# Performance work log

Measured on AMD Instinct MI355X. Metric: run time of the kernel, lower is better.

## Reference

```python
import jax, jax.numpy as jnp
import numpy as np

H = 64  # hidden_size
IN = 6  # input_size


def _uniform(key, shape, bound):
    return jax.random.uniform(key, shape, jnp.float32, -bound, bound)


def setup_inputs() -> dict:
    key = jax.random.key(0)
    ks = jax.random.split(key, 20)
    B, T = 1024, 512
    bnd = 1.0 / np.sqrt(H)  # PyTorch LSTM/Linear default init scale
    inp = {"x": jax.random.normal(ks[0], (B, T, IN), jnp.float32)}
    # LSTM params, PyTorch layout: w_ih [4H, in], w_hh [4H, H], gate order i,f,g,o
    in_sizes = [IN, H, H]
    for l in range(3):
        inp[f"w_ih{l}"] = _uniform(ks[1 + 4 * l], (4 * H, in_sizes[l]), bnd)
        inp[f"w_hh{l}"] = _uniform(ks[2 + 4 * l], (4 * H, H), bnd)
        inp[f"b_ih{l}"] = _uniform(ks[3 + 4 * l], (4 * H,), bnd)
        inp[f"b_hh{l}"] = _uniform(ks[4 + 4 * l], (4 * H,), bnd)
    # MLP head: fc1 (64->128), fc3 (128->64), fc2 (64->2)
    inp["fc1_w"] = _uniform(ks[13], (128, H), 1.0 / np.sqrt(H))
    inp["fc1_b"] = _uniform(ks[14], (128,), 1.0 / np.sqrt(H))
    inp["fc3_w"] = _uniform(ks[15], (64, 128), 1.0 / np.sqrt(128))
    inp["fc3_b"] = _uniform(ks[16], (64,), 1.0 / np.sqrt(128))
    inp["fc2_w"] = _uniform(ks[17], (2, 64), 1.0 / np.sqrt(64))
    inp["fc2_b"] = _uniform(ks[18], (2,), 1.0 / np.sqrt(64))
    return inp


def _lstm_layer(x, w_ih, w_hh, b_ih, b_hh):
    # x: [B, T, F] -> [B, T, H]; zero initial state, PyTorch gate order i,f,g,o
    B = x.shape[0]
    # Precompute input projections for all timesteps (one big GEMM)
    xg = jnp.einsum('btf,gf->btg', x, w_ih) + b_ih + b_hh  # [B, T, 4H]

    def step(carry, xt):
        h, c = carry
        gates = xt + h @ w_hh.T
        i, f, g, o = jnp.split(gates, 4, axis=-1)
        c = jax.nn.sigmoid(f) * c + jax.nn.sigmoid(i) * jnp.tanh(g)
        h = jax.nn.sigmoid(o) * jnp.tanh(c)
        return (h, c), h

    h0 = jnp.zeros((B, H), x.dtype)
    (_, _), ys = jax.lax.scan(step, (h0, h0), jnp.swapaxes(xg, 0, 1))
    return jnp.swapaxes(ys, 0, 1)


def reference(x, w_ih0, w_hh0, b_ih0, b_hh0, w_ih1, w_hh1, b_ih1, b_hh1,
              w_ih2, w_hh2, b_ih2, b_hh2, fc1_w, fc1_b, fc3_w, fc3_b, fc2_w, fc2_b):
    h = _lstm_layer(x, w_ih0, w_hh0, b_ih0, b_hh0)
    h = _lstm_layer(h, w_ih1, w_hh1, b_ih1, b_hh1)
    h = _lstm_layer(h, w_ih2, w_hh2, b_ih2, b_hh2)
    z = h[:, -1, :]  # last timestep: [B, H]
    z = jax.nn.relu(z @ fc1_w.T + fc1_b)
    z = jax.nn.relu(z @ fc3_w.T + fc3_b)
    return z @ fc2_w.T + fc2_b  # [B, 2]
```

## Files before the change

kernel.cpp:

```cpp
#include <hip/hip_runtime.h>
#include <cstdint>
#include <cstddef>

namespace {

constexpr int B_ = 1024;
constexpr int T_ = 512;
constexpr int H_ = 64;
constexpr int NG = 64;
constexpr int D_RING = 64;
constexpr int CP = 16;
constexpr int SLOT_BYTES = 16 * 64 * 2;

constexpr float L2E  = 1.4426950408889634f;

typedef short bf16x8 __attribute__((ext_vector_type(8)));
typedef float f32x4  __attribute__((ext_vector_type(4)));

__device__ __forceinline__ float exp2_hw(float x) {
    float r; asm("v_exp_f32 %0, %1" : "=v"(r) : "v"(x)); return r;
}
__device__ __forceinline__ float rcp_hw(float x) {
    float r; asm("v_rcp_f32 %0, %1" : "=v"(r) : "v"(x)); return r;
}

__device__ __forceinline__ unsigned short f2bf(float f) {
    unsigned u = __float_as_uint(f);
    u += 0x7FFF + ((u >> 16) & 1);
    return (unsigned short)(u >> 16);
}

__device__ __forceinline__ unsigned cvtpk_bf16(float a, float b) {
    unsigned r;
    asm("v_cvt_pk_bf16_f32 %0, %1, %2" : "=v"(r) : "v"(a), "v"(b));
    return r;
}

__device__ __forceinline__ void lds_barrier() {
    asm volatile("s_waitcnt lgkmcnt(0)\n\ts_barrier" ::: "memory");
}

__device__ __forceinline__ void ring_store16(void* dst, bf16x8 v) {
    asm volatile("global_store_dwordx4 %0, %1, off sc0 sc1"
                 :: "v"(dst), "v"(v) : "memory");
}
__device__ __forceinline__ int flag_load(const int* p) {
    int v;
    asm volatile("global_load_dword %0, %1, off sc0 sc1\n\t"
                 "s_waitcnt vmcnt(0)" : "=v"(v) : "v"(p) : "memory");
    return v;
}
__device__ __forceinline__ void flag_store_drain(int* p, int v) {
    asm volatile("s_waitcnt vmcnt(0)\n\t"
                 "global_store_dword %0, %1, off sc0 sc1"
                 :: "v"(p), "v"(v) : "memory");
}
__device__ __forceinline__ void flag_store(int* p, int v) {
    asm volatile("global_store_dword %0, %1, off sc0 sc1"
                 :: "v"(p), "v"(v) : "memory");
}
__device__ __forceinline__ void spin_ge(const int* p, int tgt) {
    while (flag_load(p) < tgt) __builtin_amdgcn_s_sleep(1);
}

__global__ void init_flags(int* p, int n) {
    int i = blockIdx.x * 256 + threadIdx.x;
    if (i < n) p[i] = -1;
}

__global__ void cvt_bf16_kernel(const float* __restrict__ src,
                                unsigned short* __restrict__ dst, int n) {
    int i = blockIdx.x * 256 + threadIdx.x;
    if (i < n) {
        int row = i >> 6;
        float sc = ((row >> 6) == 2) ? 2.0f * L2E : L2E;
        dst[i] = f2bf(src[i] * sc);
    }
}

__global__ void cvt_wih0_kernel(const float* __restrict__ src,
                                unsigned short* __restrict__ dst) {
    int i = blockIdx.x * 256 + threadIdx.x;
    int g = i >> 3, k = i & 7;
    float sc = ((g >> 6) == 2) ? 2.0f * L2E : L2E;
    dst[i] = (k < 6) ? f2bf(src[g * 6 + k] * sc) : (unsigned short)0;
}

__global__ void build_xpk(const float* __restrict__ x,
                          unsigned short* __restrict__ xPk) {
    int idx = blockIdx.x * 256 + threadIdx.x;
    int k = idx & 7, r = (idx >> 3) & 15, g = (idx >> 7) & 63, t = idx >> 13;
    float v = (k < 6) ? x[((size_t)(g * 16 + r) * T_ + t) * 6 + k] : 0.f;
    xPk[idx] = f2bf(v);
}

template<int LAY>
__device__ __forceinline__ void pipe_body(
    int g,
    const unsigned short* __restrict__ xPk,
    const unsigned short* __restrict__ wih,
    const unsigned short* __restrict__ whh,
    const float* __restrict__ bih, const float* __restrict__ bhh,
    const unsigned short* __restrict__ ringIn, unsigned short* __restrict__ ringOut,
    const int* progIn, int* progOut, int* consInP, const int* consOutP,
    float* __restrict__ hlast, unsigned short* lds)
{
    const int tid = threadIdx.x;
    const int l   = tid & 63;
    const int w   = tid >> 6;
    const int r16 = l & 15;
    const int kq  = l >> 4;
    const int hdim = w * 16 + r16;

    bf16x8 whh_f[4][2], wih_f[4][2];
    f32x4  bias_acc[4];
    #pragma unroll
    for (int d = 0; d < 4; ++d) {
        const int gg = d * 64 + hdim;
        const float sc = (d == 2) ? 2.0f * L2E : L2E;
        const float b = (bih[gg] + bhh[gg]) * sc;
        bias_acc[d] = f32x4{b, b, b, b};
        whh_f[d][0] = *(const bf16x8*)(whh + gg * 64 + kq * 8);
        whh_f[d][1] = *(const bf16x8*)(whh + gg * 64 + 32 + kq * 8);
        if constexpr (LAY == 0) {
            bf16x8 z = {};
            wih_f[d][0] = (kq == 0) ? *(const bf16x8*)(wih + gg * 8) : z;
            wih_f[d][1] = z;
        } else {
            wih_f[d][0] = *(const bf16x8*)(wih + gg * 64 + kq * 8);
            wih_f[d][1] = *(const bf16x8*)(wih + gg * 64 + 32 + kq * 8);
        }
    }

    char* ldsb = (char*)lds;
    const int rdA0 = r16 * 128 + (((0 + kq) ^ (r16 & 7)) << 4);
    const int rdA1 = r16 * 128 + (((4 + kq) ^ (r16 & 7)) << 4);
    int wrA[4];
    #pragma unroll
    for (int r = 0; r < 4; ++r) {
        const int row = 4 * kq + r;
        wrA[r] = row * 128 + (((hdim >> 3) ^ (row & 7)) << 4) + (hdim & 7) * 2;
    }
    const int rOffA = r16 * 128 + kq * 16;
    const int rOffB = r16 * 128 + 64 + kq * 16;

    auto xrow = [&](int t) -> const char* {
        return (const char*)xPk + (((size_t)t * NG + g) * 16 + r16) * 16;
    };

    ((uint4*)ldsb)[tid] = make_uint4(0, 0, 0, 0);
    float c[4] = {0.f, 0.f, 0.f, 0.f};
    lds_barrier();

    bf16x8 cur0 = {}, cur1 = {};
    f32x4 accA[4], accB[4];
    {
        bf16x8 x0a = {}, x0b = {};
        if constexpr (LAY > 0) {
            spin_ge(progIn, (CP - 1 < T_ - 1) ? CP - 1 : T_ - 1);
            const char* s0 = (const char*)ringIn;
            const char* s1 = (const char*)ringIn + SLOT_BYTES;
            asm volatile(
                "global_load_dwordx4 %0, %4, off sc0 sc1\n\t"
                "global_load_dwordx4 %1, %5, off sc0 sc1\n\t"
                "global_load_dwordx4 %2, %6, off sc0 sc1\n\t"
                "global_load_dwordx4 %3, %7, off sc0 sc1\n\t"
                "s_waitcnt vmcnt(0)"
                : "=v"(x0a), "=v"(x0b), "=v"(cur0), "=v"(cur1)
                : "v"(s0 + rOffA), "v"(s0 + rOffB), "v"(s1 + rOffA), "v"(s1 + rOffB)
                : "memory");
            __builtin_amdgcn_sched_barrier(0);
        } else {
            asm volatile(
                "global_load_dwordx4 %0, %2, off\n\t"
                "global_load_dwordx4 %1, %3, off\n\t"
                "s_waitcnt vmcnt(0)"
                : "=v"(x0a), "=v"(cur0)
                : "v"(xrow(0)), "v"(xrow(1))
                : "memory");
            __builtin_amdgcn_sched_barrier(0);
        }
        #pragma unroll
        for (int d = 0; d < 4; ++d) {
            accA[d] = __builtin_amdgcn_mfma_f32_16x16x32_bf16(x0a, wih_f[d][0], bias_acc[d], 0, 0, 0);
            if constexpr (LAY != 0)
                accA[d] = __builtin_amdgcn_mfma_f32_16x16x32_bf16(x0b, wih_f[d][1], accA[d], 0, 0, 0);
        }
    }

    auto step = [&](int t, int par, f32x4* accC, f32x4* accN) {
        if constexpr (LAY < 2) {
            if ((t & (CP - 1)) == 0) spin_ge(consOutP, t + CP - D_RING);
        }
        if constexpr (LAY < 2) {
            if ((t & (CP - 1)) == 1 && t > 1) {
                if (tid == 0) flag_store_drain(progOut, t - 2);
            }
        }

        const bf16x8 ha = *(const bf16x8*)(ldsb + ((par ^ 1) << 11) + rdA0);
        const bf16x8 hb = *(const bf16x8*)(ldsb + ((par ^ 1) << 11) + rdA1);

        #pragma unroll
        for (int d = 0; d < 4; ++d) {
            accC[d] = __builtin_amdgcn_mfma_f32_16x16x32_bf16(ha, whh_f[d][0], accC[d], 0, 0, 0);
            accC[d] = __builtin_amdgcn_mfma_f32_16x16x32_bf16(hb, whh_f[d][1], accC[d], 0, 0, 0);
        }

        if constexpr (LAY < 2) {
            if (w == 0) asm volatile("s_waitcnt vmcnt(2)" ::: "memory");
            else        asm volatile("s_waitcnt vmcnt(0)" ::: "memory");
        } else {
            asm volatile("s_waitcnt vmcnt(0)" ::: "memory");
        }
        __builtin_amdgcn_sched_barrier(0);

        if (t + 1 < T_) {
            #pragma unroll
            for (int d = 0; d < 4; ++d) {
                accN[d] = __builtin_amdgcn_mfma_f32_16x16x32_bf16(cur0, wih_f[d][0], bias_acc[d], 0, 0, 0);
                if constexpr (LAY != 0)
                    accN[d] = __builtin_amdgcn_mfma_f32_16x16x32_bf16(cur1, wih_f[d][1], accN[d], 0, 0, 0);
            }
        }

        {
            const int s = t + 2;
            if (s < T_) {
                if constexpr (LAY > 0) {
                    if ((s & (CP - 1)) == 0) {
                        int tgt = s + CP - 1; if (tgt > T_ - 1) tgt = T_ - 1;
                        spin_ge(progIn, tgt);
                    }
                    const char* src = (const char*)ringIn + (s & (D_RING - 1)) * SLOT_BYTES;
                    asm volatile(
                        "global_load_dwordx4 %0, %2, off sc0 sc1\n\t"
                        "global_load_dwordx4 %1, %3, off sc0 sc1"
                        : "=v"(cur0), "=v"(cur1)
                        : "v"(src + rOffA), "v"(src + rOffB)
                        : "memory");
                } else {
                    asm volatile("global_load_dwordx4 %0, %1, off"
                                 : "=v"(cur0) : "v"(xrow(s)) : "memory");
                }
            }
        }

        if constexpr (LAY < 2) {
            if (w == 0) {
                char* dst = (char*)ringOut + ((t - 1) & (D_RING - 1)) * SLOT_BYTES;
                ring_store16(dst + rOffA, ha);
                ring_store16(dst + rOffB, hb);
            }
        }

        float h[4];
        #pragma unroll
        for (int r = 0; r < 4; ++r) {
            const float gi = accC[0][r], gf = accC[1][r], gg = accC[2][r], go = accC[3][r];
            const float si = rcp_hw(1.0f + exp2_hw(-gi));
            const float sf = rcp_hw(1.0f + exp2_hw(-gf));
            const float so = rcp_hw(1.0f + exp2_hw(-go));
            const float tg = __builtin_fmaf(2.0f, rcp_hw(1.0f + exp2_hw(-gg)), -1.0f);
            c[r] = sf * c[r] + si * tg;
            const float tc = __builtin_fmaf(2.0f, rcp_hw(1.0f + exp2_hw(c[r] * (-2.0f * L2E))), -1.0f);
            h[r] = so * tc;
        }
        const unsigned p01 = cvtpk_bf16(h[0], h[1]);
        const unsigned p23 = cvtpk_bf16(h[2], h[3]);
        char* wbase = ldsb + (par << 11);
        *(unsigned short*)(wbase + wrA[0]) = (unsigned short)(p01 & 0xffff);
        *(unsigned short*)(wbase + wrA[1]) = (unsigned short)(p01 >> 16);
        *(unsigned short*)(wbase + wrA[2]) = (unsigned short)(p23 & 0xffff);
        *(unsigned short*)(wbase + wrA[3]) = (unsigned short)(p23 >> 16);
        if constexpr (LAY == 2) {
            if (t == T_ - 1) {
                #pragma unroll
                for (int r = 0; r < 4; ++r)
                    hlast[(g * 16 + kq * 4 + r) * 64 + hdim] = h[r];
            }
        }

        lds_barrier();

        if constexpr (LAY > 0) {
            if (tid == 0 && (t & (CP - 1)) == CP - 1) flag_store(consInP, t);
        }
    };

    #pragma unroll 1
    for (int t = 0; t < T_; t += 2) {
        step(t,     0, accA, accB);
        step(t + 1, 1, accB, accA);
    }

    if constexpr (LAY < 2) {
        if (w == 0) {
            const int par = (T_ - 1) & 1;
            const bf16x8 ha = *(const bf16x8*)(ldsb + (par << 11) + rdA0);
            const bf16x8 hb = *(const bf16x8*)(ldsb + (par << 11) + rdA1);
            char* dst = (char*)ringOut + ((T_ - 1) & (D_RING - 1)) * SLOT_BYTES;
            ring_store16(dst + rOffA, ha);
            ring_store16(dst + rOffB, hb);
        }
        lds_barrier();
        if (tid == 0) flag_store_drain(progOut, T_ - 1);
    }
}

__global__ __launch_bounds__(256, 1)
void lstm_pipe(const unsigned short* __restrict__ xPk,
               const unsigned short* __restrict__ wih0p,
               const unsigned short* __restrict__ wih1,
               const unsigned short* __restrict__ wih2,
               const unsigned short* __restrict__ whh0,
               const unsigned short* __restrict__ whh1,
               const unsigned short* __restrict__ whh2,
               const float* __restrict__ bih0, const float* __restrict__ bhh0,
               const float* __restrict__ bih1, const float* __restrict__ bhh1,
               const float* __restrict__ bih2, const float* __restrict__ bhh2,
               unsigned short* __restrict__ ring, int* __restrict__ flags,
               float* __restrict__ hlast)
{
    __shared__ unsigned short lds[2][1024];

    const int g   = blockIdx.x & 63;
    const int lay = blockIdx.x >> 6;

    const size_t GSHORTS = (size_t)D_RING * SLOT_BYTES / 2;
    unsigned short* r0 = ring + ((size_t)0 * NG + g) * GSHORTS;
    unsigned short* r1 = ring + ((size_t)1 * NG + g) * GSHORTS;
    int* prog0 = flags + (0 * 64 + g) * 16;
    int* prog1 = flags + (1 * 64 + g) * 16;
    int* cons0 = flags + (128 + 0 * 64 + g) * 16;
    int* cons1 = flags + (128 + 1 * 64 + g) * 16;

    if (lay == 0) {
        pipe_body<0>(g, xPk, wih0p, whh0, bih0, bhh0,
                     nullptr, r0, nullptr, prog0, nullptr, cons0,
                     hlast, &lds[0][0]);
    } else if (lay == 1) {
        pipe_body<1>(g, xPk, wih1, whh1, bih1, bhh1,
                     r0, r1, prog0, prog1, cons0, cons1,
                     hlast, &lds[0][0]);
    } else {
        pipe_body<2>(g, xPk, wih2, whh2, bih2, bhh2,
                     r1, nullptr, prog1, nullptr, cons1, nullptr,
                     hlast, &lds[0][0]);
    }
}

__global__ __launch_bounds__(128)
void mlp_head_kernel(const float* __restrict__ hlast,
                     const float* __restrict__ fc1_w, const float* __restrict__ fc1_b,
                     const float* __restrict__ fc3_w, const float* __restrict__ fc3_b,
                     const float* __restrict__ fc2_w, const float* __restrict__ fc2_b,
                     float* __restrict__ outp)
{
    __shared__ float s_h[H_];
    __shared__ float s_z1[128];
    __shared__ float s_z3[64];
    const int b = blockIdx.x, tid = threadIdx.x;

    if (tid < H_) s_h[tid] = hlast[b * H_ + tid];
    __syncthreads();

    {
        float acc = fc1_b[tid];
        #pragma unroll
        for (int k = 0; k < H_; ++k) acc += fc1_w[tid * H_ + k] * s_h[k];
        s_z1[tid] = fmaxf(acc, 0.0f);
    }
    __syncthreads();

    if (tid < 64) {
        float acc = fc3_b[tid];
        #pragma unroll
        for (int k = 0; k < 128; ++k) acc += fc3_w[tid * 128 + k] * s_z1[k];
        s_z3[tid] = fmaxf(acc, 0.0f);
    }
    __syncthreads();

    if (tid < 2) {
        float acc = fc2_b[tid];
        #pragma unroll
        for (int k = 0; k < 64; ++k) acc += fc2_w[tid * 64 + k] * s_z3[k];
        outp[b * 2 + tid] = acc;
    }
}

}

extern "C" void kernel_launch(void* const* d_in, const int* in_sizes, int n_in,
                              void* d_out, int out_size, void* d_ws, size_t ws_size,
                              hipStream_t stream) {
    (void)in_sizes; (void)n_in; (void)out_size; (void)ws_size;

    const float* x     = (const float*)d_in[0];
    const float* wih0  = (const float*)d_in[1];
    const float* whh0  = (const float*)d_in[2];
    const float* bih0  = (const float*)d_in[3];
    const float* bhh0  = (const float*)d_in[4];
    const float* wih1  = (const float*)d_in[5];
    const float* whh1  = (const float*)d_in[6];
    const float* bih1  = (const float*)d_in[7];
    const float* bhh1  = (const float*)d_in[8];
    const float* wih2  = (const float*)d_in[9];
    const float* whh2  = (const float*)d_in[10];
    const float* bih2  = (const float*)d_in[11];
    const float* bhh2  = (const float*)d_in[12];
    const float* fc1_w = (const float*)d_in[13];
    const float* fc1_b = (const float*)d_in[14];
    const float* fc3_w = (const float*)d_in[15];
    const float* fc3_b = (const float*)d_in[16];
    const float* fc2_w = (const float*)d_in[17];
    const float* fc2_b = (const float*)d_in[18];
    float* out = (float*)d_out;

    char* base = (char*)d_ws;
    const size_t RING_B = (size_t)2 * NG * D_RING * SLOT_BYTES;
    const size_t XPK_B  = (size_t)T_ * NG * 16 * 8 * 2;
    const size_t FLAG_B = 4096 * sizeof(int);
    unsigned short* ring  = (unsigned short*)(base);
    unsigned short* xPk   = (unsigned short*)(base + RING_B);
    int*            flags = (int*)(base + RING_B + XPK_B);
    float*          hlast = (float*)(base + RING_B + XPK_B + FLAG_B);
    char* wp = base + RING_B + XPK_B + FLAG_B + (size_t)B_ * H_ * 4;
    unsigned short* whh_b[3];
    for (int i = 0; i < 3; ++i) { whh_b[i] = (unsigned short*)wp; wp += 256 * 64 * 2; }
    unsigned short* wih_b1 = (unsigned short*)wp; wp += 256 * 64 * 2;
    unsigned short* wih_b2 = (unsigned short*)wp; wp += 256 * 64 * 2;
    unsigned short* wih0p  = (unsigned short*)wp; wp += 256 * 8 * 2;

    init_flags<<<16, 256, 0, stream>>>(flags, 4096);
    const int NW = 256 * 64;
    cvt_bf16_kernel<<<NW / 256, 256, 0, stream>>>(whh0, whh_b[0], NW);
    cvt_bf16_kernel<<<NW / 256, 256, 0, stream>>>(whh1, whh_b[1], NW);
    cvt_bf16_kernel<<<NW / 256, 256, 0, stream>>>(whh2, whh_b[2], NW);
    cvt_bf16_kernel<<<NW / 256, 256, 0, stream>>>(wih1, wih_b1, NW);
    cvt_bf16_kernel<<<NW / 256, 256, 0, stream>>>(wih2, wih_b2, NW);
    cvt_wih0_kernel<<<8, 256, 0, stream>>>(wih0, wih0p);
    build_xpk<<<(T_ * NG * 16 * 8) / 256, 256, 0, stream>>>(x, xPk);

    lstm_pipe<<<192, 256, 0, stream>>>(xPk, wih0p, wih_b1, wih_b2,
                                       whh_b[0], whh_b[1], whh_b[2],
                                       bih0, bhh0, bih1, bhh1, bih2, bhh2,
                                       ring, flags, hlast);

    mlp_head_kernel<<<B_, 128, 0, stream>>>(hlast, fc1_w, fc1_b, fc3_w, fc3_b,
                                            fc2_w, fc2_b, out);
}
```

Before: 393.1 us.

## Fuse three LSTM layers into one wavefront-pipelined block per batch group

Replaces the 192-block cross-block pipeline, in which each layer ran on its own block and passed hidden states through a global-memory ring guarded by spin flags, with 64 blocks that each run all three layers. The layers are skewed by one timestep and hand off hidden states through LDS tiles. This removes global ring traffic, flag polling and the flag-init kernel. In exchange each block does three layers' worth of MFMA and activation work serially per step, which lengthens the per-step critical path, and only 64 CUs are used. Register pressure also rises because all three layers' weights are held in registers.

New measurement: 793.5 us. +101.8%, slower.

```diff
diff --git a/kernel.cpp b/kernel.cpp
--- a/kernel.cpp
+++ b/kernel.cpp
@@ -8,9 +8,6 @@
 constexpr int T_ = 512;
 constexpr int H_ = 64;
 constexpr int NG = 64;
-constexpr int D_RING = 64;
-constexpr int CP = 16;
-constexpr int SLOT_BYTES = 16 * 64 * 2;
 
 constexpr float L2E  = 1.4426950408889634f;
 
@@ -40,33 +37,6 @@
     asm volatile("s_waitcnt lgkmcnt(0)\n\ts_barrier" ::: "memory");
 }
 
-__device__ __forceinline__ void ring_store16(void* dst, bf16x8 v) {
-    asm volatile("global_store_dwordx4 %0, %1, off sc0 sc1"
-                 :: "v"(dst), "v"(v) : "memory");
-}
-__device__ __forceinline__ int flag_load(const int* p) {
-    int v;
-    asm volatile("global_load_dword %0, %1, off sc0 sc1\n\t"
-                 "s_waitcnt vmcnt(0)" : "=v"(v) : "v"(p) : "memory");
-    return v;
-}
-__device__ __forceinline__ void flag_store_drain(int* p, int v) {
-    asm volatile("s_waitcnt vmcnt(0)\n\t"
-                 "global_store_dword %0, %1, off sc0 sc1"
-                 :: "v"(p), "v"(v) : "memory");
-}
-__device__ __forceinline__ void flag_store(int* p, int v) {
-    asm volatile("global_store_dword %0, %1, off sc0 sc1"
-                 :: "v"(p), "v"(v) : "memory");
-}
-__device__ __forceinline__ void spin_ge(const int* p, int tgt) {
-    while (flag_load(p) < tgt) __builtin_amdgcn_s_sleep(1);
-}
-
-__global__ void init_flags(int* p, int n) {
-    int i = blockIdx.x * 256 + threadIdx.x;
-    if (i < n) p[i] = -1;
-}
 
 __global__ void cvt_bf16_kernel(const float* __restrict__ src,
                                 unsigned short* __restrict__ dst, int n) {
@@ -94,17 +64,22 @@
     xPk[idx] = f2bf(v);
 }
 
-template<int LAY>
-__device__ __forceinline__ void pipe_body(
-    int g,
-    const unsigned short* __restrict__ xPk,
-    const unsigned short* __restrict__ wih,
-    const unsigned short* __restrict__ whh,
-    const float* __restrict__ bih, const float* __restrict__ bhh,
-    const unsigned short* __restrict__ ringIn, unsigned short* __restrict__ ringOut,
-    const int* progIn, int* progOut, int* consInP, const int* consOutP,
-    float* __restrict__ hlast, unsigned short* lds)
+__global__ __launch_bounds__(256, 1)
+void lstm_fused(const unsigned short* __restrict__ xPk,
+                const unsigned short* __restrict__ wih0p,
+                const unsigned short* __restrict__ wih1,
+                const unsigned short* __restrict__ wih2,
+                const unsigned short* __restrict__ whh0,
+                const unsigned short* __restrict__ whh1,
+                const unsigned short* __restrict__ whh2,
+                const float* __restrict__ bih0, const float* __restrict__ bhh0,
+                const float* __restrict__ bih1, const float* __restrict__ bhh1,
+                const float* __restrict__ bih2, const float* __restrict__ bhh2,
+                float* __restrict__ hlast)
 {
+    __shared__ unsigned short lds[6][1024];
+
+    const int g   = blockIdx.x;
     const int tid = threadIdx.x;
     const int l   = tid & 63;
     const int w   = tid >> 6;
@@ -112,24 +87,34 @@
     const int kq  = l >> 4;
     const int hdim = w * 16 + r16;
 
-    bf16x8 whh_f[4][2], wih_f[4][2];
-    f32x4  bias_acc[4];
+    bf16x8 w0h[4][2], w0x[4];
+    bf16x8 w1h[4][2], w1x[4][2];
+    bf16x8 w2h[4][2], w2x[4][2];
+    f32x4  b0[4], b1[4], b2[4];
     #pragma unroll
     for (int d = 0; d < 4; ++d) {
         const int gg = d * 64 + hdim;
         const float sc = (d == 2) ? 2.0f * L2E : L2E;
-        const float b = (bih[gg] + bhh[gg]) * sc;
-        bias_acc[d] = f32x4{b, b, b, b};
-        whh_f[d][0] = *(const bf16x8*)(whh + gg * 64 + kq * 8);
-        whh_f[d][1] = *(const bf16x8*)(whh + gg * 64 + 32 + kq * 8);
-        if constexpr (LAY == 0) {
+        const float v0 = (bih0[gg] + bhh0[gg]) * sc;
+        const float v1 = (bih1[gg] + bhh1[gg]) * sc;
+        const float v2 = (bih2[gg] + bhh2[gg]) * sc;
+        b0[d] = f32x4{v0, v0, v0, v0};
+        b1[d] = f32x4{v1, v1, v1, v1};
+        b2[d] = f32x4{v2, v2, v2, v2};
+        w0h[d][0] = *(const bf16x8*)(whh0 + gg * 64 + kq * 8);
+        w0h[d][1] = *(const bf16x8*)(whh0 + gg * 64 + 32 + kq * 8);
+        w1h[d][0] = *(const bf16x8*)(whh1 + gg * 64 + kq * 8);
+        w1h[d][1] = *(const bf16x8*)(whh1 + gg * 64 + 32 + kq * 8);
+        w2h[d][0] = *(const bf16x8*)(whh2 + gg * 64 + kq * 8);
+        w2h[d][1] = *(const bf16x8*)(whh2 + gg * 64 + 32 + kq * 8);
+        {
             bf16x8 z = {};
-            wih_f[d][0] = (kq == 0) ? *(const bf16x8*)(wih + gg * 8) : z;
-            wih_f[d][1] = z;
-        } else {
-            wih_f[d][0] = *(const bf16x8*)(wih + gg * 64 + kq * 8);
-            wih_f[d][1] = *(const bf16x8*)(wih + gg * 64 + 32 + kq * 8);
-        }
+            w0x[d] = (kq == 0) ? *(const bf16x8*)(wih0p + gg * 8) : z;
+        }
+        w1x[d][0] = *(const bf16x8*)(wih1 + gg * 64 + kq * 8);
+        w1x[d][1] = *(const bf16x8*)(wih1 + gg * 64 + 32 + kq * 8);
+        w2x[d][0] = *(const bf16x8*)(wih2 + gg * 64 + kq * 8);
+        w2x[d][1] = *(const bf16x8*)(wih2 + gg * 64 + 32 + kq * 8);
     }
 
     char* ldsb = (char*)lds;
@@ -141,123 +126,32 @@
         const int row = 4 * kq + r;
         wrA[r] = row * 128 + (((hdim >> 3) ^ (row & 7)) << 4) + (hdim & 7) * 2;
     }
-    const int rOffA = r16 * 128 + kq * 16;
-    const int rOffB = r16 * 128 + 64 + kq * 16;
-
-    auto xrow = [&](int t) -> const char* {
-        return (const char*)xPk + (((size_t)t * NG + g) * 16 + r16) * 16;
-    };
-
-    ((uint4*)ldsb)[tid] = make_uint4(0, 0, 0, 0);
-    float c[4] = {0.f, 0.f, 0.f, 0.f};
+    auto tile = [&](int layer, int p) -> char* {
+        return ldsb + (size_t)(layer * 2 + p) * 2048;
+    };
+
+    {
+        uint4* z = (uint4*)ldsb;
+        z[tid] = make_uint4(0, 0, 0, 0);
+        z[tid + 256] = make_uint4(0, 0, 0, 0);
+        z[tid + 512] = make_uint4(0, 0, 0, 0);
+    }
+    float c0[4] = {0.f, 0.f, 0.f, 0.f};
+    float c1[4] = {0.f, 0.f, 0.f, 0.f};
+    float c2[4] = {0.f, 0.f, 0.f, 0.f};
     lds_barrier();
 
-    bf16x8 cur0 = {}, cur1 = {};
-    f32x4 accA[4], accB[4];
-    {
-        bf16x8 x0a = {}, x0b = {};
-        if constexpr (LAY > 0) {
-            spin_ge(progIn, (CP - 1 < T_ - 1) ? CP - 1 : T_ - 1);
-            const char* s0 = (const char*)ringIn;
-            const char* s1 = (const char*)ringIn + SLOT_BYTES;
-            asm volatile(
-                "global_load_dwordx4 %0, %4, off sc0 sc1\n\t"
-                "global_load_dwordx4 %1, %5, off sc0 sc1\n\t"
-                "global_load_dwordx4 %2, %6, off sc0 sc1\n\t"
-                "global_load_dwordx4 %3, %7, off sc0 sc1\n\t"
-                "s_waitcnt vmcnt(0)"
-                : "=v"(x0a), "=v"(x0b), "=v"(cur0), "=v"(cur1)
-                : "v"(s0 + rOffA), "v"(s0 + rOffB), "v"(s1 + rOffA), "v"(s1 + rOffB)
-                : "memory");
-            __builtin_amdgcn_sched_barrier(0);
-        } else {
-            asm volatile(
-                "global_load_dwordx4 %0, %2, off\n\t"
-                "global_load_dwordx4 %1, %3, off\n\t"
-                "s_waitcnt vmcnt(0)"
-                : "=v"(x0a), "=v"(cur0)
-                : "v"(xrow(0)), "v"(xrow(1))
-                : "memory");
-            __builtin_amdgcn_sched_barrier(0);
-        }
-        #pragma unroll
-        for (int d = 0; d < 4; ++d) {
-            accA[d] = __builtin_amdgcn_mfma_f32_16x16x32_bf16(x0a, wih_f[d][0], bias_acc[d], 0, 0, 0);
-            if constexpr (LAY != 0)
-                accA[d] = __builtin_amdgcn_mfma_f32_16x16x32_bf16(x0b, wih_f[d][1], accA[d], 0, 0, 0);
-        }
-    }
-
-    auto step = [&](int t, int par, f32x4* accC, f32x4* accN) {
-        if constexpr (LAY < 2) {
-            if ((t & (CP - 1)) == 0) spin_ge(consOutP, t + CP - D_RING);
-        }
-        if constexpr (LAY < 2) {
-            if ((t & (CP - 1)) == 1 && t > 1) {
-                if (tid == 0) flag_store_drain(progOut, t - 2);
-            }
-        }
-
-        const bf16x8 ha = *(const bf16x8*)(ldsb + ((par ^ 1) << 11) + rdA0);
-        const bf16x8 hb = *(const bf16x8*)(ldsb + ((par ^ 1) << 11) + rdA1);
-
-        #pragma unroll
-        for (int d = 0; d < 4; ++d) {
-            accC[d] = __builtin_amdgcn_mfma_f32_16x16x32_bf16(ha, whh_f[d][0], accC[d], 0, 0, 0);
-            accC[d] = __builtin_amdgcn_mfma_f32_16x16x32_bf16(hb, whh_f[d][1], accC[d], 0, 0, 0);
-        }
-
-        if constexpr (LAY < 2) {
-            if (w == 0) asm volatile("s_waitcnt vmcnt(2)" ::: "memory");
-            else        asm volatile("s_waitcnt vmcnt(0)" ::: "memory");
-        } else {
-            asm volatile("s_waitcnt vmcnt(0)" ::: "memory");
-        }
-        __builtin_amdgcn_sched_barrier(0);
-
-        if (t + 1 < T_) {
-            #pragma unroll
-            for (int d = 0; d < 4; ++d) {
-                accN[d] = __builtin_amdgcn_mfma_f32_16x16x32_bf16(cur0, wih_f[d][0], bias_acc[d], 0, 0, 0);
-                if constexpr (LAY != 0)
-                    accN[d] = __builtin_amdgcn_mfma_f32_16x16x32_bf16(cur1, wih_f[d][1], accN[d], 0, 0, 0);
-            }
-        }
-
-        {
-            const int s = t + 2;
-            if (s < T_) {
-                if constexpr (LAY > 0) {
-                    if ((s & (CP - 1)) == 0) {
-                        int tgt = s + CP - 1; if (tgt > T_ - 1) tgt = T_ - 1;
-                        spin_ge(progIn, tgt);
-                    }
-                    const char* src = (const char*)ringIn + (s & (D_RING - 1)) * SLOT_BYTES;
-                    asm volatile(
-                        "global_load_dwordx4 %0, %2, off sc0 sc1\n\t"
-                        "global_load_dwordx4 %1, %3, off sc0 sc1"
-                        : "=v"(cur0), "=v"(cur1)
-                        : "v"(src + rOffA), "v"(src + rOffB)
-                        : "memory");
-                } else {
-                    asm volatile("global_load_dwordx4 %0, %1, off"
-                                 : "=v"(cur0) : "v"(xrow(s)) : "memory");
-                }
-            }
-        }
-
-        if constexpr (LAY < 2) {
-            if (w == 0) {
-                char* dst = (char*)ringOut + ((t - 1) & (D_RING - 1)) * SLOT_BYTES;
-                ring_store16(dst + rOffA, ha);
-                ring_store16(dst + rOffB, hb);
-            }
-        }
-
-        float h[4];
+    constexpr size_t XSTEP = (size_t)NG * 16 * 16;
+    const char* xp0 = (const char*)xPk + ((size_t)g * 16 + r16) * 16;
+    const char* xpA = xp0;
+    const char* xpB = xp0 + XSTEP;
+    bf16x8 curA = *(const bf16x8*)xpA;
+    bf16x8 curB = *(const bf16x8*)xpB;
+
+    auto cell_core = [&](const f32x4* acc, float* c, float* h) {
         #pragma unroll
         for (int r = 0; r < 4; ++r) {
-            const float gi = accC[0][r], gf = accC[1][r], gg = accC[2][r], go = accC[3][r];
+            const float gi = acc[0][r], gf = acc[1][r], gg = acc[2][r], go = acc[3][r];
             const float si = rcp_hw(1.0f + exp2_hw(-gi));
             const float sf = rcp_hw(1.0f + exp2_hw(-gf));
             const float so = rcp_hw(1.0f + exp2_hw(-go));
@@ -266,87 +160,90 @@
             const float tc = __builtin_fmaf(2.0f, rcp_hw(1.0f + exp2_hw(c[r] * (-2.0f * L2E))), -1.0f);
             h[r] = so * tc;
         }
+    };
+    auto cell_write = [&](const f32x4* acc, float* c, char* wbase) {
+        float h[4];
+        cell_core(acc, c, h);
         const unsigned p01 = cvtpk_bf16(h[0], h[1]);
         const unsigned p23 = cvtpk_bf16(h[2], h[3]);
-        char* wbase = ldsb + (par << 11);
         *(unsigned short*)(wbase + wrA[0]) = (unsigned short)(p01 & 0xffff);
         *(unsigned short*)(wbase + wrA[1]) = (unsigned short)(p01 >> 16);
         *(unsigned short*)(wbase + wrA[2]) = (unsigned short)(p23 & 0xffff);
         *(unsigned short*)(wbase + wrA[3]) = (unsigned short)(p23 >> 16);
-        if constexpr (LAY == 2) {
-            if (t == T_ - 1) {
-                #pragma unroll
-                for (int r = 0; r < 4; ++r)
-                    hlast[(g * 16 + kq * 4 + r) * 64 + hdim] = h[r];
+    };
+
+    auto L0_body = [&](int P, const bf16x8& curX) {
+        const bf16x8 ha = *(const bf16x8*)(tile(0, P ^ 1) + rdA0);
+        const bf16x8 hb = *(const bf16x8*)(tile(0, P ^ 1) + rdA1);
+        f32x4 acc[4];
+        #pragma unroll
+        for (int d = 0; d < 4; ++d) {
+            acc[d] = __builtin_amdgcn_mfma_f32_16x16x32_bf16(curX, w0x[d], b0[d], 0, 0, 0);
+            acc[d] = __builtin_amdgcn_mfma_f32_16x16x32_bf16(ha, w0h[d][0], acc[d], 0, 0, 0);
+            acc[d] = __builtin_amdgcn_mfma_f32_16x16x32_bf16(hb, w0h[d][1], acc[d], 0, 0, 0);
+        }
+        cell_write(acc, c0, tile(0, P));
+    };
+    auto L1_body = [&](int P) {
+        const bf16x8 xa = *(const bf16x8*)(tile(0, P ^ 1) + rdA0);
+        const bf16x8 xb = *(const bf16x8*)(tile(0, P ^ 1) + rdA1);
+        const bf16x8 ha = *(const bf16x8*)(tile(1, P ^ 1) + rdA0);
+        const bf16x8 hb = *(const bf16x8*)(tile(1, P ^ 1) + rdA1);
+        f32x4 acc[4];
+        #pragma unroll
+        for (int d = 0; d < 4; ++d) {
+            acc[d] = __builtin_amdgcn_mfma_f32_16x16x32_bf16(xa, w1x[d][0], b1[d], 0, 0, 0);
+            acc[d] = __builtin_amdgcn_mfma_f32_16x16x32_bf16(xb, w1x[d][1], acc[d], 0, 0, 0);
+            acc[d] = __builtin_amdgcn_mfma_f32_16x16x32_bf16(ha, w1h[d][0], acc[d], 0, 0, 0);
+            acc[d] = __builtin_amdgcn_mfma_f32_16x16x32_bf16(hb, w1h[d][1], acc[d], 0, 0, 0);
+        }
+        cell_write(acc, c1, tile(1, P));
+    };
+    auto L2_body = [&](int P, bool last) {
+        const bf16x8 xa = *(const bf16x8*)(tile(1, P ^ 1) + rdA0);
+        const bf16x8 xb = *(const bf16x8*)(tile(1, P ^ 1) + rdA1);
+        const bf16x8 ha = *(const bf16x8*)(tile(2, P ^ 1) + rdA0);
+        const bf16x8 hb = *(const bf16x8*)(tile(2, P ^ 1) + rdA1);
+        f32x4 acc[4];
+        #pragma unroll
+        for (int d = 0; d < 4; ++d) {
+            acc[d] = __builtin_amdgcn_mfma_f32_16x16x32_bf16(xa, w2x[d][0], b2[d], 0, 0, 0);
+            acc[d] = __builtin_amdgcn_mfma_f32_16x16x32_bf16(xb, w2x[d][1], acc[d], 0, 0, 0);
+            acc[d] = __builtin_amdgcn_mfma_f32_16x16x32_bf16(ha, w2h[d][0], acc[d], 0, 0, 0);
+            acc[d] = __builtin_amdgcn_mfma_f32_16x16x32_bf16(hb, w2h[d][1], acc[d], 0, 0, 0);
+        }
+        if (last) {
+            float h[4];
+            cell_core(acc, c2, h);
+            #pragma unroll
+            for (int r = 0; r < 4; ++r)
+                hlast[(g * 16 + kq * 4 + r) * 64 + hdim] = h[r];
+        } else {
+            cell_write(acc, c2, tile(2, P));
+        }
+    };
+
+    auto do_iter = [&](int i, int P, bf16x8& curX, const char*& xp) {
+        if (i >= 2 && i < T_) {
+            L0_body(P, curX);
+            if (i + 2 < T_) { xp += 2 * XSTEP; curX = *(const bf16x8*)xp; }
+            L1_body(P);
+            L2_body(P, false);
+        } else {
+            if (i < T_) {
+                L0_body(P, curX);
+                if (i + 2 < T_) { xp += 2 * XSTEP; curX = *(const bf16x8*)xp; }
             }
-        }
-
+            if (i >= 1 && i <= T_) L1_body(P);
+            if (i >= 2) L2_body(P, i == T_ + 1);
+        }
         lds_barrier();
-
-        if constexpr (LAY > 0) {
-            if (tid == 0 && (t & (CP - 1)) == CP - 1) flag_store(consInP, t);
-        }
     };
 
     #pragma unroll 1
-    for (int t = 0; t < T_; t += 2) {
-        step(t,     0, accA, accB);
-        step(t + 1, 1, accB, accA);
-    }
-
-    if constexpr (LAY < 2) {
-        if (w == 0) {
-            const int par = (T_ - 1) & 1;
-            const bf16x8 ha = *(const bf16x8*)(ldsb + (par << 11) + rdA0);
-            const bf16x8 hb = *(const bf16x8*)(ldsb + (par << 11) + rdA1);
-            char* dst = (char*)ringOut + ((T_ - 1) & (D_RING - 1)) * SLOT_BYTES;
-            ring_store16(dst + rOffA, ha);
-            ring_store16(dst + rOffB, hb);
-        }
-        lds_barrier();
-        if (tid == 0) flag_store_drain(progOut, T_ - 1);
-    }
-}
-
-__global__ __launch_bounds__(256, 1)
-void lstm_pipe(const unsigned short* __restrict__ xPk,
-               const unsigned short* __restrict__ wih0p,
-               const unsigned short* __restrict__ wih1,
-               const unsigned short* __restrict__ wih2,
-               const unsigned short* __restrict__ whh0,
-               const unsigned short* __restrict__ whh1,
-               const unsigned short* __restrict__ whh2,
-               const float* __restrict__ bih0, const float* __restrict__ bhh0,
-               const float* __restrict__ bih1, const float* __restrict__ bhh1,
-               const float* __restrict__ bih2, const float* __restrict__ bhh2,
-               unsigned short* __restrict__ ring, int* __restrict__ flags,
-               float* __restrict__ hlast)
-{
-    __shared__ unsigned short lds[2][1024];
-
-    const int g   = blockIdx.x & 63;
-    const int lay = blockIdx.x >> 6;
-
-    const size_t GSHORTS = (size_t)D_RING * SLOT_BYTES / 2;
-    unsigned short* r0 = ring + ((size_t)0 * NG + g) * GSHORTS;
-    unsigned short* r1 = ring + ((size_t)1 * NG + g) * GSHORTS;
-    int* prog0 = flags + (0 * 64 + g) * 16;
-    int* prog1 = flags + (1 * 64 + g) * 16;
-    int* cons0 = flags + (128 + 0 * 64 + g) * 16;
-    int* cons1 = flags + (128 + 1 * 64 + g) * 16;
-
-    if (lay == 0) {
-        pipe_body<0>(g, xPk, wih0p, whh0, bih0, bhh0,
-                     nullptr, r0, nullptr, prog0, nullptr, cons0,
-                     hlast, &lds[0][0]);
-    } else if (lay == 1) {
-        pipe_body<1>(g, xPk, wih1, whh1, bih1, bhh1,
-                     r0, r1, prog0, prog1, cons0, cons1,
-                     hlast, &lds[0][0]);
-    } else {
-        pipe_body<2>(g, xPk, wih2, whh2, bih2, bhh2,
-                     r1, nullptr, prog1, nullptr, cons1, nullptr,
-                     hlast, &lds[0][0]);
+    for (int i = 0; i < T_ + 2; i += 2) {
+        do_iter(i,     0, curA, xpA);
+        do_iter(i + 1, 1, curB, xpB);
     }
 }
 
@@ -418,21 +315,16 @@
     float* out = (float*)d_out;
 
     char* base = (char*)d_ws;
-    const size_t RING_B = (size_t)2 * NG * D_RING * SLOT_BYTES;
-    const size_t XPK_B  = (size_t)T_ * NG * 16 * 8 * 2;
-    const size_t FLAG_B = 4096 * sizeof(int);
-    unsigned short* ring  = (unsigned short*)(base);
-    unsigned short* xPk   = (unsigned short*)(base + RING_B);
-    int*            flags = (int*)(base + RING_B + XPK_B);
-    float*          hlast = (float*)(base + RING_B + XPK_B + FLAG_B);
-    char* wp = base + RING_B + XPK_B + FLAG_B + (size_t)B_ * H_ * 4;
+    const size_t XPK_B = (size_t)T_ * NG * 16 * 8 * 2;
+    unsigned short* xPk  = (unsigned short*)base;
+    float*          hlast = (float*)(base + XPK_B);
+    char* wp = base + XPK_B + (size_t)B_ * H_ * 4;
     unsigned short* whh_b[3];
     for (int i = 0; i < 3; ++i) { whh_b[i] = (unsigned short*)wp; wp += 256 * 64 * 2; }
     unsigned short* wih_b1 = (unsigned short*)wp; wp += 256 * 64 * 2;
     unsigned short* wih_b2 = (unsigned short*)wp; wp += 256 * 64 * 2;
     unsigned short* wih0p  = (unsigned short*)wp; wp += 256 * 8 * 2;
 
-    init_flags<<<16, 256, 0, stream>>>(flags, 4096);
     const int NW = 256 * 64;
     cvt_bf16_kernel<<<NW / 256, 256, 0, stream>>>(whh0, whh_b[0], NW);
     cvt_bf16_kernel<<<NW / 256, 256, 0, stream>>>(whh1, whh_b[1], NW);
@@ -442,10 +334,10 @@
     cvt_wih0_kernel<<<8, 256, 0, stream>>>(wih0, wih0p);
     build_xpk<<<(T_ * NG * 16 * 8) / 256, 256, 0, stream>>>(x, xPk);
 
-    lstm_pipe<<<192, 256, 0, stream>>>(xPk, wih0p, wih_b1, wih_b2,
+    lstm_fused<<<64, 256, 0, stream>>>(xPk, wih0p, wih_b1, wih_b2,
                                        whh_b[0], whh_b[1], whh_b[2],
                                        bih0, bhh0, bih1, bhh1, bih2, bhh2,
-                                       ring, flags, hlast);
+                                       hlast);
 
     mlp_head_kernel<<<B_, 128, 0, stream>>>(hlast, fc1_w, fc1_b, fc3_w, fc3_b,
                                             fc2_w, fc2_b, out);
```
